# Kernel optimization log

Measured on AMD Instinct MI355X. Metric: run time of the kernel, lower is better.

## Reference

```python
import jax, jax.numpy as jnp
import numpy as np

B, N = 1, 512
CS, CZ, H, CH, PQ, PV = 384, 128, 12, 16, 4, 8
INF, EPS = 1e5, 1e-8
SOFTPLUS_INV_1 = 0.541324854612918


def _init_linear(key, fan_in, fan_out):
    kw, kb = jax.random.split(key)
    std = float(1.0 / np.sqrt(fan_in))
    w = jax.random.normal(kw, (fan_in, fan_out), dtype=jnp.float32) * std
    b = jnp.zeros((fan_out,), dtype=jnp.float32)
    return w, b


def setup_inputs() -> dict:
    key = jax.random.key(0)
    ks = jax.random.split(key, 12)
    s = jax.random.normal(ks[0], (B, N, CS), dtype=jnp.float32)
    z = jax.random.normal(ks[1], (B, N, N, CZ), dtype=jnp.float32) * 0.1
    # proper rotation matrices via QR of random Gaussians
    rot, _ = jnp.linalg.qr(jax.random.normal(ks[2], (B, N, 3, 3), dtype=jnp.float32))
    trans = jax.random.normal(ks[3], (B, N, 3), dtype=jnp.float32) * 10.0
    mask = jnp.ones((B, N), dtype=jnp.float32)
    w_q, b_q = _init_linear(ks[4], CS, H * CH)
    w_kv, b_kv = _init_linear(ks[5], CS, 2 * H * CH)
    w_qp, b_qp = _init_linear(ks[6], CS, H * PQ * 3)
    w_kvp, b_kvp = _init_linear(ks[7], CS, H * (PQ + PV) * 3)
    w_b, b_b = _init_linear(ks[8], CZ, H)
    head_weights = jnp.full((H,), SOFTPLUS_INV_1, dtype=jnp.float32)
    concat_dim = H * (CZ + CH + PV * 4)
    # 'final' init -> zeros
    w_out = jnp.zeros((concat_dim, CS), dtype=jnp.float32)
    b_out = jnp.zeros((CS,), dtype=jnp.float32)
    return dict(s=s, z=z, rot=rot, trans=trans, mask=mask,
                w_q=w_q, b_q=b_q, w_kv=w_kv, b_kv=b_kv,
                w_qp=w_qp, b_qp=b_qp, w_kvp=w_kvp, b_kvp=b_kvp,
                w_b=w_b, b_b=b_b, head_weights=head_weights,
                w_out=w_out, b_out=b_out)


def reference(s, z, rot, trans, mask,
              w_q, b_q, w_kv, b_kv, w_qp, b_qp, w_kvp, b_kvp,
              w_b, b_b, head_weights, w_out, b_out):
    # scalar q/k/v: [B,N,H,CH]
    q = (s @ w_q + b_q).reshape(B, N, H, CH)
    kv = (s @ w_kv + b_kv).reshape(B, N, H, 2 * CH)
    k, v = kv[..., :CH], kv[..., CH:]

    def make_points(w, b, P):
        p = s @ w + b                                   # [B,N,3*H*P] (x|y|z chunks)
        p = jnp.moveaxis(p.reshape(B, N, 3, H * P), -2, -1)  # [B,N,H*P,3]
        p = jnp.einsum('bnij,bnpj->bnpi', rot, p) + trans[:, :, None]  # global frame
        return p.reshape(B, N, H, P, 3)

    q_pts = make_points(w_qp, b_qp, PQ)                 # [B,N,H,PQ,3]
    kv_pts = make_points(w_kvp, b_kvp, PQ + PV)
    k_pts, v_pts = kv_pts[..., :PQ, :], kv_pts[..., PQ:, :]

    # scalar QK attention + pair bias
    a = jnp.einsum('bqhc,bkhc->bhqk', q, k) * float(np.sqrt(1.0 / (3 * CH)))
    b_bias = z @ w_b + b_b                              # [B,N,N,H]
    a = a + float(np.sqrt(1.0 / 3.0)) * jnp.moveaxis(b_bias, -1, -3)

    # squared point-distance attention
    d = q_pts[:, :, None] - k_pts[:, None]              # [B,N,N,H,PQ,3]
    pt_att = jnp.sum(d * d, axis=-1)                    # [B,N,N,H,PQ]
    hw = jax.nn.softplus(head_weights) * float(np.sqrt(1.0 / (3 * (PQ * 9.0 / 2))))
    pt_att = -0.5 * jnp.sum(pt_att * hw[None, None, None, :, None], axis=-1)  # [B,N,N,H]
    a = a + jnp.moveaxis(pt_att, -1, -3)                # [B,H,N,N]

    sq_mask = (mask[:, :, None] * mask[:, None, :] - 1.0) * INF
    a = jax.nn.softmax(a + sq_mask[:, None], axis=-1)   # [B,H,N,N]

    # standard value path
    o = jnp.einsum('bhqk,bkhc->bqhc', a, v).reshape(B, N, H * CH)
    # point value path, rotated back to local frame
    o_pt = jnp.einsum('bhqk,bkhpc->bqhpc', a, v_pts)    # [B,N,H,PV,3]
    o_pt = jnp.einsum('bnji,bnhpj->bnhpi', rot, o_pt - trans[:, :, None, None])
    o_pt_norm = jnp.sqrt(jnp.sum(o_pt ** 2, axis=-1) + EPS).reshape(B, N, H * PV)
    o_pt = o_pt.reshape(B, N, H * PV, 3)
    # pair-weighted path
    o_pair = jnp.einsum('bhqk,bqkc->bqhc', a, z).reshape(B, N, H * CZ)

    o_cat = jnp.concatenate(
        [o, o_pt[..., 0], o_pt[..., 1], o_pt[..., 2], o_pt_norm, o_pair], axis=-1)
    return o_cat @ w_out + b_out
```

## Files before the change

### kernel.cpp

```cpp
#include <hip/hip_runtime.h>
#include <math.h>

#define NRES 512
#define CSD  384
#define CZD  128

#define OFF_Q     0
#define OFF_KT    98304
#define OFF_VC    196608
#define OFF_QP    458752
#define OFF_KPT   532480
#define OFF_A     606208
#define OFF_OCAT  3751936
#define OFF_WCAT  4833280
#define OFF_BCAT  (OFF_WCAT + 442368)
#define OFF_PRAWQ OFF_A
#define OFF_PRAWK (OFF_A + 73728)
#define OFF_PART  OFF_A

__global__ __launch_bounds__(256) void k_wcat(
    const float* __restrict__ w_q, const float* __restrict__ b_q,
    const float* __restrict__ w_kv, const float* __restrict__ b_kv,
    const float* __restrict__ w_qp, const float* __restrict__ b_qp,
    const float* __restrict__ w_kvp, const float* __restrict__ b_kvp,
    float* __restrict__ wcat, float* __restrict__ bcat)
{
    const int idx = blockIdx.x * 256 + threadIdx.x;
    if (idx < 442368) {
        const int k = idx / 1152, c = idx % 1152;
        float v;
        if (c < 192)      v = w_q[k*192 + c];
        else if (c < 576) v = w_kv[k*384 + (c - 192)];
        else if (c < 720) v = w_qp[k*144 + (c - 576)];
        else              v = w_kvp[k*432 + (c - 720)];
        wcat[idx] = v;
    } else if (idx < 443520) {
        const int c = idx - 442368;
        float v;
        if (c < 192)      v = b_q[c];
        else if (c < 576) v = b_kv[c - 192];
        else if (c < 720) v = b_qp[c - 576];
        else              v = b_kvp[c - 720];
        bcat[c] = v;
    }
}

__global__ __launch_bounds__(256) void k_proj2(
    const float* __restrict__ s, const float* __restrict__ wcat, const float* __restrict__ bcat,
    float* __restrict__ q, float* __restrict__ kkT, float* __restrict__ vcomb,
    float* __restrict__ praw_q, float* __restrict__ praw_kv)
{
    const int ct = blockIdx.x;
    const int n0 = blockIdx.y * 32;
    const int t = threadIdx.x;

    __shared__ float sT[32][34];
    __shared__ float wt[32][36];

    const int lr = t >> 3, lc4 = t & 7;
    const int tr = t >> 4, tc = t & 15;
    float4 sv4, wv4;

    sv4 = *(const float4*)&s[(n0 + lr) * CSD + lc4 * 4];
    wv4 = *(const float4*)&wcat[lr * 1152 + ct * 32 + lc4 * 4];
    sT[lc4*4+0][lr] = sv4.x; sT[lc4*4+1][lr] = sv4.y; sT[lc4*4+2][lr] = sv4.z; sT[lc4*4+3][lr] = sv4.w;
    *(float4*)&wt[lr][lc4*4] = wv4;
    __syncthreads();

    float a00 = 0.f, a01 = 0.f, a10 = 0.f, a11 = 0.f;

    for (int it = 0; it < 12; ++it) {
        if (it < 11) {
            const int k0 = (it + 1) * 32;
            sv4 = *(const float4*)&s[(n0 + lr) * CSD + k0 + lc4 * 4];
            wv4 = *(const float4*)&wcat[(k0 + lr) * 1152 + ct * 32 + lc4 * 4];
        }
        #pragma unroll
        for (int kx = 0; kx < 32; ++kx) {
            float2 ss = *(const float2*)&sT[kx][tr * 2];
            float2 ww = *(const float2*)&wt[kx][tc * 2];
            a00 += ss.x * ww.x; a01 += ss.x * ww.y;
            a10 += ss.y * ww.x; a11 += ss.y * ww.y;
        }
        __syncthreads();
        if (it < 11) {
            sT[lc4*4+0][lr] = sv4.x; sT[lc4*4+1][lr] = sv4.y; sT[lc4*4+2][lr] = sv4.z; sT[lc4*4+3][lr] = sv4.w;
            *(float4*)&wt[lr][lc4*4] = wv4;
            __syncthreads();
        }
    }

    float accv[2][2] = {{a00, a01}, {a10, a11}};
    #pragma unroll
    for (int i = 0; i < 2; ++i) {
        const int n = n0 + tr * 2 + i;
        #pragma unroll
        for (int j = 0; j < 2; ++j) {
            const int gcol = ct * 32 + tc * 2 + j;
            const float v = accv[i][j] + bcat[gcol];
            if (gcol < 192) {
                q[n*192 + gcol] = v;
            } else if (gcol < 576) {
                int g = gcol - 192, h = g >> 5, cc = g & 31;
                if (cc < 16) kkT[(h*16 + cc)*NRES + n] = v;
                else         vcomb[n*NRES + h*16 + (cc-16)] = v;
            } else if (gcol < 720) {
                praw_q[n*144 + (gcol - 576)] = v;
            } else {
                praw_kv[n*432 + (gcol - 720)] = v;
            }
        }
    }
}

__global__ __launch_bounds__(256) void k_rot(
    const float* __restrict__ praw_q, const float* __restrict__ praw_kv,
    const float* __restrict__ rot, const float* __restrict__ trans,
    float* __restrict__ q_pts, float* __restrict__ kptsT, float* __restrict__ vcomb)
{
    const int idx = blockIdx.x * 256 + threadIdx.x;
    const int n = idx / 192, u = idx % 192;
    const float* R = rot + n*9;
    const float* T = trans + n*3;
    float px, py, pz;
    if (u < 48) {
        px = praw_q[n*144 + u]; py = praw_q[n*144 + 48 + u]; pz = praw_q[n*144 + 96 + u];
    } else {
        int pt = u - 48;
        px = praw_kv[n*432 + pt]; py = praw_kv[n*432 + 144 + pt]; pz = praw_kv[n*432 + 288 + pt];
    }
    float x  = R[0]*px + R[1]*py + R[2]*pz + T[0];
    float y  = R[3]*px + R[4]*py + R[5]*pz + T[1];
    float zc = R[6]*px + R[7]*py + R[8]*pz + T[2];
    if (u < 48) {
        int o = (n*48 + u)*3;
        q_pts[o] = x; q_pts[o+1] = y; q_pts[o+2] = zc;
    } else {
        int pt = u - 48;
        int h = pt / 12, pp = pt % 12;
        if (pp < 4) {
            int dim = (h*4 + pp)*3;
            kptsT[(dim+0)*NRES + n] = x;
            kptsT[(dim+1)*NRES + n] = y;
            kptsT[(dim+2)*NRES + n] = zc;
        } else {
            int u2 = (h*8 + (pp-4))*3;
            vcomb[n*NRES + 192 + u2+0] = x;
            vcomb[n*NRES + 192 + u2+1] = y;
            vcomb[n*NRES + 192 + u2+2] = zc;
        }
    }
}

__global__ __launch_bounds__(256) void k_bias(
    const float* __restrict__ z, const float* __restrict__ w_b, const float* __restrict__ b_b,
    float* __restrict__ biasT)
{
    const int qn = blockIdx.y;
    const int k0 = blockIdx.x * 64;
    const int t = threadIdx.x;
    __shared__ float zt[64*129];
    __shared__ float wb[128*12];
    __shared__ float part[4][64][13];

    for (int i = t; i < 1536; i += 256) wb[i] = w_b[i];
    const float4* zp4 = (const float4*)(z + ((size_t)qn*NRES + k0)*CZD);
    #pragma unroll
    for (int r = 0; r < 8; ++r) {
        int idx = t + r*256;
        int kx = idx >> 5, c4 = idx & 31;
        float4 v4 = zp4[idx];
        float* dst = &zt[kx*129 + c4*4];
        dst[0] = v4.x; dst[1] = v4.y; dst[2] = v4.z; dst[3] = v4.w;
    }
    __syncthreads();

    const int kx = t & 63, qr = t >> 6;
    float acc[12];
    #pragma unroll
    for (int h = 0; h < 12; ++h) acc[h] = 0.f;
    const float* zrow = &zt[kx*129 + qr*32];
    const float* wbp = &wb[qr*32*12];
    for (int c = 0; c < 32; ++c) {
        float zv = zrow[c];
        #pragma unroll
        for (int h = 0; h < 12; ++h) acc[h] += zv * wbp[c*12 + h];
    }
    #pragma unroll
    for (int h = 0; h < 12; ++h) part[qr][kx][h] = acc[h];
    __syncthreads();

    for (int d = t; d < 768; d += 256) {
        int h = d >> 6, k2 = d & 63;
        float b = b_b[h] + part[0][k2][h] + part[1][k2][h] + part[2][k2][h] + part[3][k2][h];
        biasT[(size_t)h*NRES*NRES + (size_t)qn*NRES + k0 + k2] = b;
    }
}

__global__ __launch_bounds__(256) void k_logits(
    const float* __restrict__ q, const float* __restrict__ kkT,
    const float* __restrict__ q_pts, const float* __restrict__ kptsT,
    const float* __restrict__ head_weights, const float* __restrict__ mask,
    float* __restrict__ aT)
{
    const int qn = blockIdx.x, h = blockIdx.y;
    const int t = threadIdx.x;
    const int lane = t & 63, wv = t >> 6;
    __shared__ float red[4];

    const float hw = logf(1.f + expf(head_weights[h])) * 0.13608276f;
    const float mq = mask[qn];
    float qv[16], qpv[12];
    #pragma unroll
    for (int c = 0; c < 16; ++c) qv[c] = q[qn*192 + h*16 + c];
    #pragma unroll
    for (int d = 0; d < 12; ++d) qpv[d] = q_pts[qn*144 + h*12 + d];

    float* arow = aT + (size_t)h*NRES*NRES + (size_t)qn*NRES;
    const float* kT  = kkT + h*16*NRES;
    const float* kpT = kptsT + h*12*NRES;

    float l[2];
    #pragma unroll
    for (int r = 0; r < 2; ++r) {
        const int kn = t + r*256;
        float acc = 0.f;
        #pragma unroll
        for (int c = 0; c < 16; ++c) acc += qv[c] * kT[c*NRES + kn];
        acc *= 0.14433757f;
        acc += 0.57735027f * arow[kn];
        float dsum = 0.f;
        #pragma unroll
        for (int d = 0; d < 12; ++d) {
            float df = qpv[d] - kpT[d*NRES + kn];
            dsum += df*df;
        }
        l[r] = acc - 0.5f * hw * dsum + (mq * mask[kn] - 1.f) * 100000.f;
    }

    float m = fmaxf(l[0], l[1]);
    #pragma unroll
    for (int off = 32; off > 0; off >>= 1) m = fmaxf(m, __shfl_xor(m, off));
    if (lane == 0) red[wv] = m;
    __syncthreads();
    m = fmaxf(fmaxf(red[0], red[1]), fmaxf(red[2], red[3]));
    __syncthreads();
    float e0 = __expf(l[0] - m), e1 = __expf(l[1] - m);
    float ss = e0 + e1;
    #pragma unroll
    for (int off = 32; off > 0; off >>= 1) ss += __shfl_xor(ss, off);
    if (lane == 0) red[wv] = ss;
    __syncthreads();
    const float inv = 1.f / (red[0] + red[1] + red[2] + red[3]);
    arow[t]       = e0 * inv;
    arow[t + 256] = e1 * inv;
}

__global__ __launch_bounds__(256) void k_pair(
    const float* __restrict__ aT, const float* __restrict__ z, float* __restrict__ o_cat)
{
    const int qn = blockIdx.x;
    const int t = threadIdx.x;
    __shared__ float a_lds[12][521];
    __shared__ float part[4][12][128];

    for (int i = t; i < 12*NRES; i += 256)
        a_lds[i >> 9][i & 511] = aT[(size_t)(i >> 9)*NRES*NRES + (size_t)qn*NRES + (i & 511)];
    __syncthreads();

    const int c4 = t & 31, kgrp = t >> 5;
    const float4* zp = (const float4*)(z + (size_t)qn*NRES*CZD) + c4;
    float4 acc4[12];
    #pragma unroll
    for (int h = 0; h < 12; ++h) acc4[h] = make_float4(0.f,0.f,0.f,0.f);

    #pragma unroll 4
    for (int kn = kgrp; kn < NRES; kn += 8) {
        float4 zv = zp[kn*32];
        #pragma unroll
        for (int h = 0; h < 12; ++h) {
            float av = a_lds[h][kn];
            acc4[h].x += av*zv.x; acc4[h].y += av*zv.y;
            acc4[h].z += av*zv.z; acc4[h].w += av*zv.w;
        }
    }
    #pragma unroll
    for (int h = 0; h < 12; ++h) {
        acc4[h].x += __shfl_xor(acc4[h].x, 32);
        acc4[h].y += __shfl_xor(acc4[h].y, 32);
        acc4[h].z += __shfl_xor(acc4[h].z, 32);
        acc4[h].w += __shfl_xor(acc4[h].w, 32);
    }
    const int wave = t >> 6;
    if ((t & 63) < 32) {
        #pragma unroll
        for (int h = 0; h < 12; ++h) {
            part[wave][h][c4*4+0] = acc4[h].x;
            part[wave][h][c4*4+1] = acc4[h].y;
            part[wave][h][c4*4+2] = acc4[h].z;
            part[wave][h][c4*4+3] = acc4[h].w;
        }
    }
    __syncthreads();
    for (int i = t; i < 1536; i += 256) {
        int h = i >> 7, c = i & 127;
        float v = part[0][h][c] + part[1][h][c] + part[2][h][c] + part[3][h][c];
        o_cat[qn*2112 + 576 + h*128 + c] = v;
    }
}

__global__ __launch_bounds__(512) void k_epi(
    const float* __restrict__ aT, const float* __restrict__ vcomb,
    const float* __restrict__ rot, const float* __restrict__ trans,
    float* __restrict__ o_cat)
{
    const int qn = blockIdx.x;
    const int t = threadIdx.x;
    __shared__ float a_lds[12][521];
    __shared__ float optraw[288];

    for (int i = t; i < 12*NRES; i += 512)
        a_lds[i >> 9][i & 511] = aT[(size_t)(i >> 9)*NRES*NRES + (size_t)qn*NRES + (i & 511)];
    __syncthreads();

    const int h = (t < 192) ? (t >> 4) : ((t < 480) ? (t - 192) / 24 : 0);
    const float* vp = vcomb + t;
    float acc = 0.f;
    #pragma unroll 8
    for (int kn = 0; kn < NRES; ++kn)
        acc += a_lds[h][kn] * vp[(size_t)kn*NRES];

    if (t < 192)            o_cat[qn*2112 + t] = acc;
    else if (t < 480)       optraw[t - 192] = acc;
    __syncthreads();

    if (t < 96) {
        const float* R = rot + qn*9;
        const float* T = trans + qn*3;
        float ox = optraw[t*3]   - T[0];
        float oy = optraw[t*3+1] - T[1];
        float oz = optraw[t*3+2] - T[2];
        float x  = R[0]*ox + R[3]*oy + R[6]*oz;
        float y  = R[1]*ox + R[4]*oy + R[7]*oz;
        float zc = R[2]*ox + R[5]*oy + R[8]*oz;
        float* ob = o_cat + qn*2112;
        ob[192 + t] = x;
        ob[288 + t] = y;
        ob[384 + t] = zc;
        ob[480 + t] = sqrtf(x*x + y*y + zc*zc + 1e-8f);
    }
}

__global__ __launch_bounds__(256) void k_out2(
    const float* __restrict__ o_cat, const float* __restrict__ w_out, float* __restrict__ part)
{
    const int ct = blockIdx.x;
    const int n0 = blockIdx.y * 32;
    const int kc = blockIdx.z;
    const int t = threadIdx.x;

    __shared__ float oT[32][34];
    __shared__ float wt[32][36];

    const int lr = t >> 3, lc4 = t & 7;
    const int tr = t >> 4, tc = t & 15;
    const int kbase = kc * 352;
    float4 ov4, wv4;

    ov4 = *(const float4*)&o_cat[(n0 + lr) * 2112 + kbase + lc4 * 4];
    wv4 = *(const float4*)&w_out[(kbase + lr) * 384 + ct * 32 + lc4 * 4];
    oT[lc4*4+0][lr] = ov4.x; oT[lc4*4+1][lr] = ov4.y; oT[lc4*4+2][lr] = ov4.z; oT[lc4*4+3][lr] = ov4.w;
    *(float4*)&wt[lr][lc4*4] = wv4;
    __syncthreads();

    float a00 = 0.f, a01 = 0.f, a10 = 0.f, a11 = 0.f;

    for (int it = 0; it < 11; ++it) {
        if (it < 10) {
            const int k0 = kbase + (it + 1) * 32;
            ov4 = *(const float4*)&o_cat[(n0 + lr) * 2112 + k0 + lc4 * 4];
            wv4 = *(const float4*)&w_out[(k0 + lr) * 384 + ct * 32 + lc4 * 4];
        }
        #pragma unroll
        for (int kx = 0; kx < 32; ++kx) {
            float2 oo = *(const float2*)&oT[kx][tr * 2];
            float2 ww = *(const float2*)&wt[kx][tc * 2];
            a00 += oo.x * ww.x; a01 += oo.x * ww.y;
            a10 += oo.y * ww.x; a11 += oo.y * ww.y;
        }
        __syncthreads();
        if (it < 10) {
            oT[lc4*4+0][lr] = ov4.x; oT[lc4*4+1][lr] = ov4.y; oT[lc4*4+2][lr] = ov4.z; oT[lc4*4+3][lr] = ov4.w;
            *(float4*)&wt[lr][lc4*4] = wv4;
            __syncthreads();
        }
    }

    float* pp = part + (size_t)kc * 196608;
    pp[(n0 + tr*2 + 0)*384 + ct*32 + tc*2 + 0] = a00;
    pp[(n0 + tr*2 + 0)*384 + ct*32 + tc*2 + 1] = a01;
    pp[(n0 + tr*2 + 1)*384 + ct*32 + tc*2 + 0] = a10;
    pp[(n0 + tr*2 + 1)*384 + ct*32 + tc*2 + 1] = a11;
}

__global__ __launch_bounds__(256) void k_red(
    const float* __restrict__ part, const float* __restrict__ b_out, float* __restrict__ out)
{
    const int i = blockIdx.x*256 + threadIdx.x;
    float acc = b_out[i % 384];
    #pragma unroll
    for (int dc = 0; dc < 6; ++dc) acc += part[(size_t)dc*196608 + i];
    out[i] = acc;
}

extern "C" void kernel_launch(void* const* d_in, const int* in_sizes, int n_in,
                              void* d_out, int out_size, void* d_ws, size_t ws_size,
                              hipStream_t stream) {
    (void)in_sizes; (void)n_in; (void)out_size; (void)ws_size;
    const float* s      = (const float*)d_in[0];
    const float* z      = (const float*)d_in[1];
    const float* rot    = (const float*)d_in[2];
    const float* trans  = (const float*)d_in[3];
    const float* mask   = (const float*)d_in[4];
    const float* w_q    = (const float*)d_in[5];
    const float* b_q    = (const float*)d_in[6];
    const float* w_kv   = (const float*)d_in[7];
    const float* b_kv   = (const float*)d_in[8];
    const float* w_qp   = (const float*)d_in[9];
    const float* b_qp   = (const float*)d_in[10];
    const float* w_kvp  = (const float*)d_in[11];
    const float* b_kvp  = (const float*)d_in[12];
    const float* w_b    = (const float*)d_in[13];
    const float* b_b    = (const float*)d_in[14];
    const float* hwts   = (const float*)d_in[15];
    const float* w_out  = (const float*)d_in[16];
    const float* b_out  = (const float*)d_in[17];
    float* out = (float*)d_out;
    float* ws  = (float*)d_ws;

    float* q      = ws + OFF_Q;
    float* kkT    = ws + OFF_KT;
    float* vcomb  = ws + OFF_VC;
    float* qp     = ws + OFF_QP;
    float* kptsT  = ws + OFF_KPT;
    float* aT     = ws + OFF_A;
    float* ocat   = ws + OFF_OCAT;
    float* wcat   = ws + OFF_WCAT;
    float* bcat   = ws + OFF_BCAT;
    float* part   = ws + OFF_PART;
    float* praw_q  = ws + OFF_PRAWQ;
    float* praw_kv = ws + OFF_PRAWK;

    k_wcat<<<dim3(1733), dim3(256), 0, stream>>>(w_q, b_q, w_kv, b_kv, w_qp, b_qp, w_kvp, b_kvp, wcat, bcat);
    k_proj2<<<dim3(36, 16), dim3(256), 0, stream>>>(s, wcat, bcat, q, kkT, vcomb, praw_q, praw_kv);
    k_rot<<<dim3(384), dim3(256), 0, stream>>>(praw_q, praw_kv, rot, trans, qp, kptsT, vcomb);
    k_bias<<<dim3(8, NRES), dim3(256), 0, stream>>>(z, w_b, b_b, aT);
    k_logits<<<dim3(NRES, 12), dim3(256), 0, stream>>>(q, kkT, qp, kptsT, hwts, mask, aT);
    k_pair<<<dim3(NRES), dim3(256), 0, stream>>>(aT, z, ocat);
    k_epi<<<dim3(NRES), dim3(512), 0, stream>>>(aT, vcomb, rot, trans, ocat);
    k_out2<<<dim3(12, 16, 6), dim3(256), 0, stream>>>(ocat, w_out, part);
    k_red<<<dim3(768), dim3(256), 0, stream>>>(part, b_out, out);
}
```

Baseline: 166.7 us.

## Fuse bias, logits, softmax, pair and value paths into one per-row kernel

Four kernels (pair bias, logits+softmax, pair-weighted output, value/point epilogue) are merged into a single kernel with one block per query residue that keeps the 12x512 attention row in LDS. This removes the 12x512x512 attention matrix round trip through global memory and three launches. The cost is only 512 blocks of 256 threads with heavy LDS use (about 60KB), which limits occupancy. The bias stage now runs serially over 8 key tiles inside one block instead of across 4096 blocks.

Result: faster. 149.8 us (-10.2%).

```diff
diff --git a/kernel.cpp b/kernel.cpp
--- a/kernel.cpp
+++ b/kernel.cpp
@@ -152,186 +152,177 @@
     }
 }
 
-__global__ __launch_bounds__(256) void k_bias(
-    const float* __restrict__ z, const float* __restrict__ w_b, const float* __restrict__ b_b,
-    float* __restrict__ biasT)
-{
-    const int qn = blockIdx.y;
-    const int k0 = blockIdx.x * 64;
+__global__ __launch_bounds__(256) void k_row(
+    const float* __restrict__ z,
+    const float* __restrict__ q, const float* __restrict__ kkT, const float* __restrict__ vcomb,
+    const float* __restrict__ q_pts, const float* __restrict__ kptsT,
+    const float* __restrict__ w_b, const float* __restrict__ b_b,
+    const float* __restrict__ head_weights, const float* __restrict__ mask,
+    const float* __restrict__ rot, const float* __restrict__ trans,
+    float* __restrict__ o_cat)
+{
+    const int qn = blockIdx.x;
     const int t = threadIdx.x;
+
     __shared__ float zt[64*129];
     __shared__ float wb[128*12];
     __shared__ float part[4][64][13];
+    __shared__ float a_lds[12][520];
+    __shared__ float q_lds[192];
+    __shared__ float qp_lds[144];
+    __shared__ float hw_lds[12];
+    __shared__ float optraw[288];
 
     for (int i = t; i < 1536; i += 256) wb[i] = w_b[i];
-    const float4* zp4 = (const float4*)(z + ((size_t)qn*NRES + k0)*CZD);
-    #pragma unroll
-    for (int r = 0; r < 8; ++r) {
-        int idx = t + r*256;
-        int kx = idx >> 5, c4 = idx & 31;
-        float4 v4 = zp4[idx];
-        float* dst = &zt[kx*129 + c4*4];
-        dst[0] = v4.x; dst[1] = v4.y; dst[2] = v4.z; dst[3] = v4.w;
-    }
-    __syncthreads();
+    if (t < 192) q_lds[t] = q[qn*192 + t];
+    if (t < 144) qp_lds[t] = q_pts[qn*144 + t];
+    if (t < 12)  hw_lds[t] = logf(1.f + expf(head_weights[t])) * 0.13608276f;
 
     const int kx = t & 63, qr = t >> 6;
-    float acc[12];
-    #pragma unroll
-    for (int h = 0; h < 12; ++h) acc[h] = 0.f;
-    const float* zrow = &zt[kx*129 + qr*32];
-    const float* wbp = &wb[qr*32*12];
-    for (int c = 0; c < 32; ++c) {
-        float zv = zrow[c];
-        #pragma unroll
-        for (int h = 0; h < 12; ++h) acc[h] += zv * wbp[c*12 + h];
-    }
-    #pragma unroll
-    for (int h = 0; h < 12; ++h) part[qr][kx][h] = acc[h];
-    __syncthreads();
-
-    for (int d = t; d < 768; d += 256) {
-        int h = d >> 6, k2 = d & 63;
-        float b = b_b[h] + part[0][k2][h] + part[1][k2][h] + part[2][k2][h] + part[3][k2][h];
-        biasT[(size_t)h*NRES*NRES + (size_t)qn*NRES + k0 + k2] = b;
-    }
-}
-
-__global__ __launch_bounds__(256) void k_logits(
-    const float* __restrict__ q, const float* __restrict__ kkT,
-    const float* __restrict__ q_pts, const float* __restrict__ kptsT,
-    const float* __restrict__ head_weights, const float* __restrict__ mask,
-    float* __restrict__ aT)
-{
-    const int qn = blockIdx.x, h = blockIdx.y;
-    const int t = threadIdx.x;
-    const int lane = t & 63, wv = t >> 6;
-    __shared__ float red[4];
-
-    const float hw = logf(1.f + expf(head_weights[h])) * 0.13608276f;
+    for (int kt = 0; kt < 8; ++kt) {
+        const int k0 = kt*64;
+        __syncthreads();
+        const float4* zp4 = (const float4*)(z + ((size_t)qn*NRES + k0)*CZD);
+        #pragma unroll
+        for (int r = 0; r < 8; ++r) {
+            int idx = t + r*256;
+            int kk2 = idx >> 5, c4 = idx & 31;
+            float4 v4 = zp4[idx];
+            float* dst = &zt[kk2*129 + c4*4];
+            dst[0]=v4.x; dst[1]=v4.y; dst[2]=v4.z; dst[3]=v4.w;
+        }
+        __syncthreads();
+        float acc[12];
+        #pragma unroll
+        for (int h = 0; h < 12; ++h) acc[h] = 0.f;
+        const float* zrow = &zt[kx*129 + qr*32];
+        const float* wbp = &wb[qr*32*12];
+        for (int c = 0; c < 32; ++c) {
+            float zv = zrow[c];
+            #pragma unroll
+            for (int h = 0; h < 12; ++h) acc[h] += zv * wbp[c*12+h];
+        }
+        #pragma unroll
+        for (int h = 0; h < 12; ++h) part[qr][kx][h] = acc[h];
+        __syncthreads();
+        for (int d = t; d < 768; d += 256) {
+            int h = d >> 6, k2 = d & 63;
+            a_lds[h][k0+k2] = b_b[h] + part[0][k2][h] + part[1][k2][h]
+                            + part[2][k2][h] + part[3][k2][h];
+        }
+    }
+    __syncthreads();
+
     const float mq = mask[qn];
-    float qv[16], qpv[12];
-    #pragma unroll
-    for (int c = 0; c < 16; ++c) qv[c] = q[qn*192 + h*16 + c];
-    #pragma unroll
-    for (int d = 0; d < 12; ++d) qpv[d] = q_pts[qn*144 + h*12 + d];
-
-    float* arow = aT + (size_t)h*NRES*NRES + (size_t)qn*NRES;
-    const float* kT  = kkT + h*16*NRES;
-    const float* kpT = kptsT + h*12*NRES;
-
-    float l[2];
-    #pragma unroll
-    for (int r = 0; r < 2; ++r) {
-        const int kn = t + r*256;
-        float acc = 0.f;
-        #pragma unroll
-        for (int c = 0; c < 16; ++c) acc += qv[c] * kT[c*NRES + kn];
-        acc *= 0.14433757f;
-        acc += 0.57735027f * arow[kn];
-        float dsum = 0.f;
-        #pragma unroll
-        for (int d = 0; d < 12; ++d) {
-            float df = qpv[d] - kpT[d*NRES + kn];
-            dsum += df*df;
-        }
-        l[r] = acc - 0.5f * hw * dsum + (mq * mask[kn] - 1.f) * 100000.f;
-    }
-
-    float m = fmaxf(l[0], l[1]);
-    #pragma unroll
-    for (int off = 32; off > 0; off >>= 1) m = fmaxf(m, __shfl_xor(m, off));
-    if (lane == 0) red[wv] = m;
-    __syncthreads();
-    m = fmaxf(fmaxf(red[0], red[1]), fmaxf(red[2], red[3]));
-    __syncthreads();
-    float e0 = __expf(l[0] - m), e1 = __expf(l[1] - m);
-    float ss = e0 + e1;
-    #pragma unroll
-    for (int off = 32; off > 0; off >>= 1) ss += __shfl_xor(ss, off);
-    if (lane == 0) red[wv] = ss;
-    __syncthreads();
-    const float inv = 1.f / (red[0] + red[1] + red[2] + red[3]);
-    arow[t]       = e0 * inv;
-    arow[t + 256] = e1 * inv;
-}
-
-__global__ __launch_bounds__(256) void k_pair(
-    const float* __restrict__ aT, const float* __restrict__ z, float* __restrict__ o_cat)
-{
-    const int qn = blockIdx.x;
-    const int t = threadIdx.x;
-    __shared__ float a_lds[12][521];
-    __shared__ float part[4][12][128];
-
-    for (int i = t; i < 12*NRES; i += 256)
-        a_lds[i >> 9][i & 511] = aT[(size_t)(i >> 9)*NRES*NRES + (size_t)qn*NRES + (i & 511)];
-    __syncthreads();
-
-    const int c4 = t & 31, kgrp = t >> 5;
-    const float4* zp = (const float4*)(z + (size_t)qn*NRES*CZD) + c4;
-    float4 acc4[12];
-    #pragma unroll
-    for (int h = 0; h < 12; ++h) acc4[h] = make_float4(0.f,0.f,0.f,0.f);
-
-    #pragma unroll 4
-    for (int kn = kgrp; kn < NRES; kn += 8) {
-        float4 zv = zp[kn*32];
+    for (int h = 0; h < 12; ++h) {
+        float qv[16], qpv[12];
+        #pragma unroll
+        for (int c = 0; c < 16; ++c) qv[c] = q_lds[h*16+c];
+        #pragma unroll
+        for (int d = 0; d < 12; ++d) qpv[d] = qp_lds[h*12+d];
+        const float hw = hw_lds[h];
+        const float* kT  = kkT + h*16*NRES;
+        const float* kpT = kptsT + h*12*NRES;
+        #pragma unroll
+        for (int r = 0; r < 2; ++r) {
+            const int kn = t + r*256;
+            float acc = 0.f;
+            #pragma unroll
+            for (int c = 0; c < 16; ++c) acc += qv[c] * kT[c*NRES + kn];
+            acc *= 0.14433757f;
+            acc += 0.57735027f * a_lds[h][kn];
+            float dsum = 0.f;
+            #pragma unroll
+            for (int d = 0; d < 12; ++d) { float df = qpv[d] - kpT[d*NRES + kn]; dsum += df*df; }
+            a_lds[h][kn] = acc - 0.5f*hw*dsum + (mq*mask[kn]-1.f)*100000.f;
+        }
+    }
+    __syncthreads();
+
+    {
+        const int w = t >> 6, lane = t & 63;
+        for (int h = w; h < 12; h += 4) {
+            float m = -1e30f;
+            #pragma unroll
+            for (int i = 0; i < 8; ++i) m = fmaxf(m, a_lds[h][lane + i*64]);
+            #pragma unroll
+            for (int off = 32; off > 0; off >>= 1) m = fmaxf(m, __shfl_xor(m, off));
+            float ss = 0.f;
+            #pragma unroll
+            for (int i = 0; i < 8; ++i) {
+                float e = __expf(a_lds[h][lane + i*64] - m);
+                a_lds[h][lane + i*64] = e;
+                ss += e;
+            }
+            #pragma unroll
+            for (int off = 32; off > 0; off >>= 1) ss += __shfl_xor(ss, off);
+            float inv = 1.f / ss;
+            #pragma unroll
+            for (int i = 0; i < 8; ++i) a_lds[h][lane + i*64] *= inv;
+        }
+    }
+    __syncthreads();
+
+    {
+        const int c4 = t & 31, kgrp = t >> 5;
+        const float4* zp = (const float4*)(z + (size_t)qn*NRES*CZD) + c4;
+        float4 acc4[12];
+        #pragma unroll
+        for (int h = 0; h < 12; ++h) acc4[h] = make_float4(0.f,0.f,0.f,0.f);
+
+        #pragma unroll 4
+        for (int kn = kgrp; kn < NRES; kn += 8) {
+            float4 zv = zp[kn*32];
+            #pragma unroll
+            for (int h = 0; h < 12; ++h) {
+                float av = a_lds[h][kn];
+                acc4[h].x += av*zv.x; acc4[h].y += av*zv.y;
+                acc4[h].z += av*zv.z; acc4[h].w += av*zv.w;
+            }
+        }
         #pragma unroll
         for (int h = 0; h < 12; ++h) {
-            float av = a_lds[h][kn];
-            acc4[h].x += av*zv.x; acc4[h].y += av*zv.y;
-            acc4[h].z += av*zv.z; acc4[h].w += av*zv.w;
-        }
-    }
-    #pragma unroll
-    for (int h = 0; h < 12; ++h) {
-        acc4[h].x += __shfl_xor(acc4[h].x, 32);
-        acc4[h].y += __shfl_xor(acc4[h].y, 32);
-        acc4[h].z += __shfl_xor(acc4[h].z, 32);
-        acc4[h].w += __shfl_xor(acc4[h].w, 32);
-    }
-    const int wave = t >> 6;
-    if ((t & 63) < 32) {
-        #pragma unroll
-        for (int h = 0; h < 12; ++h) {
-            part[wave][h][c4*4+0] = acc4[h].x;
-            part[wave][h][c4*4+1] = acc4[h].y;
-            part[wave][h][c4*4+2] = acc4[h].z;
-            part[wave][h][c4*4+3] = acc4[h].w;
-        }
-    }
-    __syncthreads();
-    for (int i = t; i < 1536; i += 256) {
-        int h = i >> 7, c = i & 127;
-        float v = part[0][h][c] + part[1][h][c] + part[2][h][c] + part[3][h][c];
-        o_cat[qn*2112 + 576 + h*128 + c] = v;
-    }
-}
-
-__global__ __launch_bounds__(512) void k_epi(
-    const float* __restrict__ aT, const float* __restrict__ vcomb,
-    const float* __restrict__ rot, const float* __restrict__ trans,
-    float* __restrict__ o_cat)
-{
-    const int qn = blockIdx.x;
-    const int t = threadIdx.x;
-    __shared__ float a_lds[12][521];
-    __shared__ float optraw[288];
-
-    for (int i = t; i < 12*NRES; i += 512)
-        a_lds[i >> 9][i & 511] = aT[(size_t)(i >> 9)*NRES*NRES + (size_t)qn*NRES + (i & 511)];
-    __syncthreads();
-
-    const int h = (t < 192) ? (t >> 4) : ((t < 480) ? (t - 192) / 24 : 0);
-    const float* vp = vcomb + t;
-    float acc = 0.f;
-    #pragma unroll 8
-    for (int kn = 0; kn < NRES; ++kn)
-        acc += a_lds[h][kn] * vp[(size_t)kn*NRES];
-
-    if (t < 192)            o_cat[qn*2112 + t] = acc;
-    else if (t < 480)       optraw[t - 192] = acc;
+            acc4[h].x += __shfl_xor(acc4[h].x, 32);
+            acc4[h].y += __shfl_xor(acc4[h].y, 32);
+            acc4[h].z += __shfl_xor(acc4[h].z, 32);
+            acc4[h].w += __shfl_xor(acc4[h].w, 32);
+        }
+        float (*ppart)[12][128] = (float (*)[12][128])zt;
+        const int wave = t >> 6;
+        if ((t & 63) < 32) {
+            #pragma unroll
+            for (int h = 0; h < 12; ++h) {
+                ppart[wave][h][c4*4+0] = acc4[h].x;
+                ppart[wave][h][c4*4+1] = acc4[h].y;
+                ppart[wave][h][c4*4+2] = acc4[h].z;
+                ppart[wave][h][c4*4+3] = acc4[h].w;
+            }
+        }
+        __syncthreads();
+        for (int i = t; i < 1536; i += 256) {
+            int h = i >> 7, c = i & 127;
+            float v = ppart[0][h][c] + ppart[1][h][c] + ppart[2][h][c] + ppart[3][h][c];
+            o_cat[qn*2112 + 576 + h*128 + c] = v;
+        }
+    }
+
+    {
+        const int u0 = t;
+        const int h0 = (u0 < 192) ? (u0 >> 4) : (u0 - 192) / 24;
+        const int u1v = (t < 224) ? (t + 256) : 479;
+        const int h1 = (u1v - 192) / 24;
+        float acc0 = 0.f, acc1 = 0.f;
+        const float* vp = vcomb;
+        #pragma unroll 8
+        for (int kn = 0; kn < NRES; ++kn) {
+            const float* row = vp + (size_t)kn*NRES;
+            acc0 += a_lds[h0][kn] * row[u0];
+            acc1 += a_lds[h1][kn] * row[u1v];
+        }
+        if (u0 < 192) o_cat[qn*2112 + u0] = acc0;
+        else          optraw[u0 - 192] = acc0;
+        if (t < 224)  optraw[t + 64] = acc1;
+    }
     __syncthreads();
 
     if (t < 96) {
@@ -443,7 +434,6 @@
     float* vcomb  = ws + OFF_VC;
     float* qp     = ws + OFF_QP;
     float* kptsT  = ws + OFF_KPT;
-    float* aT     = ws + OFF_A;
     float* ocat   = ws + OFF_OCAT;
     float* wcat   = ws + OFF_WCAT;
     float* bcat   = ws + OFF_BCAT;
@@ -454,10 +444,8 @@
     k_wcat<<<dim3(1733), dim3(256), 0, stream>>>(w_q, b_q, w_kv, b_kv, w_qp, b_qp, w_kvp, b_kvp, wcat, bcat);
     k_proj2<<<dim3(36, 16), dim3(256), 0, stream>>>(s, wcat, bcat, q, kkT, vcomb, praw_q, praw_kv);
     k_rot<<<dim3(384), dim3(256), 0, stream>>>(praw_q, praw_kv, rot, trans, qp, kptsT, vcomb);
-    k_bias<<<dim3(8, NRES), dim3(256), 0, stream>>>(z, w_b, b_b, aT);
-    k_logits<<<dim3(NRES, 12), dim3(256), 0, stream>>>(q, kkT, qp, kptsT, hwts, mask, aT);
-    k_pair<<<dim3(NRES), dim3(256), 0, stream>>>(aT, z, ocat);
-    k_epi<<<dim3(NRES), dim3(512), 0, stream>>>(aT, vcomb, rot, trans, ocat);
+    k_row<<<dim3(NRES), dim3(256), 0, stream>>>(z, q, kkT, vcomb, qp, kptsT,
+        w_b, b_b, hwts, mask, rot, trans, ocat);
     k_out2<<<dim3(12, 16, 6), dim3(256), 0, stream>>>(ocat, w_out, part);
     k_red<<<dim3(768), dim3(256), 0, stream>>>(part, b_out, out);
 }
```
